# Performance work log

Hardware: AMD Instinct MI355X
Metric: run time of the kernel (lower is better)

Reference implementation:

```python
import jax, jax.numpy as jnp
import numpy as np
import math
from itertools import combinations

SEQ_LEN = 8
SET_SIZE = 3
IN_DIM = 2048
OUT_DIM = 1152
WAY = 5
SHOT = 5
N_QUERIES = 200
PE_SCALE = 0.1
LN_EPS = 1e-5
NEG_INF = -1e30

TUPLES = np.array(list(combinations(range(SEQ_LEN), SET_SIZE)), dtype=np.int32)  # [56, 3]
TUPLES_LEN = TUPLES.shape[0]


def _positional_encoding(d_model, max_len):
    position = np.arange(max_len)[:, None].astype(np.float32)
    div_term = np.exp(np.arange(0, d_model, 2).astype(np.float32) * -(math.log(10000.0) / d_model))
    pe = np.zeros((max_len, d_model), dtype=np.float32)
    pe[:, 0::2] = np.sin(position * div_term) * PE_SCALE
    pe[:, 1::2] = np.cos(position * div_term) * PE_SCALE
    return jnp.asarray(pe)

PE = _positional_encoding(IN_DIM, int(SEQ_LEN * 1.5))


def setup_inputs() -> dict:
    key = jax.random.key(0)
    ks = jax.random.split(key, 6)
    support_set = jax.random.normal(ks[0], (WAY * SHOT, SEQ_LEN, IN_DIM), dtype=jnp.float32)
    queries = jax.random.normal(ks[1], (N_QUERIES, SEQ_LEN, IN_DIM), dtype=jnp.float32)
    support_labels = jnp.repeat(jnp.arange(WAY, dtype=jnp.int32), SHOT)  # [25]
    Wk = jax.random.normal(ks[2], (IN_DIM * SET_SIZE, OUT_DIM), dtype=jnp.float32) * 0.02
    bk = jnp.zeros((OUT_DIM,), dtype=jnp.float32)
    Wv = jax.random.normal(ks[3], (IN_DIM * SET_SIZE, OUT_DIM), dtype=jnp.float32) * 0.02
    bv = jnp.zeros((OUT_DIM,), dtype=jnp.float32)
    ln_g = jnp.ones((OUT_DIM,), dtype=jnp.float32)
    ln_b = jnp.zeros((OUT_DIM,), dtype=jnp.float32)
    return {"support_set": support_set, "support_labels": support_labels, "queries": queries,
            "Wk": Wk, "bk": bk, "Wv": Wv, "bv": bv, "ln_g": ln_g, "ln_b": ln_b}


def _layernorm(x, g, b):
    mu = jnp.mean(x, axis=-1, keepdims=True)
    var = jnp.var(x, axis=-1, keepdims=True)
    return (x - mu) * jax.lax.rsqrt(var + LN_EPS) * g + b


def _tuple_features(x):
    # x: [N, SEQ_LEN, IN_DIM]; add PE (dropout is identity at inference), gather frame tuples.
    n = x.shape[0]
    x = x + PE[None, :x.shape[1], :]
    return x[:, TUPLES, :].reshape(n, TUPLES_LEN, SET_SIZE * IN_DIM)  # [N, 56, 6144]


def reference(support_set, support_labels, queries, Wk, bk, Wv, bv, ln_g, ln_b):
    n_q = queries.shape[0]
    s_feat = _tuple_features(support_set)   # [S, T, 6144]
    q_feat = _tuple_features(queries)       # [Q, T, 6144]

    sk = _layernorm(s_feat @ Wk + bk, ln_g, ln_b)  # [S, T, D]
    qk = _layernorm(q_feat @ Wk + bk, ln_g, ln_b)  # [Q, T, D]
    sv = s_feat @ Wv + bv                           # [S, T, D]
    qv = q_feat @ Wv + bv                           # [Q, T, D]

    # scores between every query tuple and every support tuple
    scores = jnp.einsum('qtd,skd->qtsk', qk, sk) / math.sqrt(OUT_DIM)  # [Q, T, S, T]

    # per-class masked softmax over (support clips of class c) x (support tuples)
    class_mask = support_labels[None, :] == jnp.arange(WAY, dtype=support_labels.dtype)[:, None]  # [WAY, S]
    masked = scores[None] + jnp.where(class_mask[:, None, None, :, None], 0.0, NEG_INF)  # [WAY, Q, T, S, T]
    attn = jax.nn.softmax(masked.reshape(WAY, n_q, TUPLES_LEN, -1), axis=-1)
    attn = attn.reshape(WAY, n_q, TUPLES_LEN, -1, TUPLES_LEN)  # [WAY, Q, T, S, T]

    proto = jnp.einsum('cqtsk,skd->cqtd', attn, sv)  # [WAY, Q, T, D]
    diff = qv[None] - proto                           # [WAY, Q, T, D]
    dist = -jnp.sum(diff * diff, axis=(2, 3)) / TUPLES_LEN  # [WAY, Q]
    return dist.T  # logits [Q, WAY]
```

## Files before the change

kernel.cpp:

```cpp
#include <hip/hip_runtime.h>
#include <math.h>

#define SEQ_LEN 8
#define IN_DIM 2048
#define OUT_DIM 1152
#define NTUP 56
#define NSUP 25
#define NQ 200
#define WAY 5
#define SFRAMES 200
#define NFRAMES 1800
#define SROWS 1400
#define QROWS 11200
#define AT_STRIDE 1440
#define KC 288
#define ALD 296

typedef __attribute__((ext_vector_type(8))) short short8;
typedef __attribute__((ext_vector_type(4))) float f32x4;

__device__ __constant__ int TUP[NTUP][3] = {
{0,1,2},{0,1,3},{0,1,4},{0,1,5},{0,1,6},{0,1,7},
{0,2,3},{0,2,4},{0,2,5},{0,2,6},{0,2,7},
{0,3,4},{0,3,5},{0,3,6},{0,3,7},
{0,4,5},{0,4,6},{0,4,7},
{0,5,6},{0,5,7},
{0,6,7},
{1,2,3},{1,2,4},{1,2,5},{1,2,6},{1,2,7},
{1,3,4},{1,3,5},{1,3,6},{1,3,7},
{1,4,5},{1,4,6},{1,4,7},
{1,5,6},{1,5,7},
{1,6,7},
{2,3,4},{2,3,5},{2,3,6},{2,3,7},
{2,4,5},{2,4,6},{2,4,7},
{2,5,6},{2,5,7},
{2,6,7},
{3,4,5},{3,4,6},{3,4,7},
{3,5,6},{3,5,7},
{3,6,7},
{4,5,6},{4,5,7},
{4,6,7},
{5,6,7}};

__device__ __forceinline__ unsigned short f2bf(float x) {
  union { float f; unsigned int u; } v; v.f = x;
  unsigned int r = v.u + 0x7fffu + ((v.u >> 16) & 1u);
  return (unsigned short)(r >> 16);
}
__device__ __forceinline__ float bf2f(unsigned short s) {
  union { float f; unsigned int u; } v; v.u = ((unsigned int)s) << 16;
  return v.f;
}

__device__ __forceinline__ void gll16(const void* g, void* l) {
  __builtin_amdgcn_global_load_lds(
      (const __attribute__((address_space(1))) unsigned int*)g,
      (__attribute__((address_space(3))) unsigned int*)l, 16, 0, 0);
}

#define VMCNT(N) asm volatile("s_waitcnt vmcnt(" #N ")" ::: "memory")

__device__ __forceinline__ void pbar() {
  asm volatile("" ::: "memory");
  __builtin_amdgcn_s_barrier();
  asm volatile("" ::: "memory");
}

#define APB_OFF   0UL
#define WT_OFF    7372800UL
#define PB_OFF    35684352UL
#define QKB_OFF   60567552UL
#define SKB_OFF   86372352UL
#define QVB_OFF   89597952UL
#define SVB_OFF   115402752UL
#define G2_OFF    118628352UL
#define SCB_OFF   119457792UL
#define G1B_OFF   151713792UL
#define QNORM_OFF 183969792UL
#define RANK_OFF  184014592UL

__global__ __launch_bounds__(256) void k_pre(const float* __restrict__ S,
                                             const float* __restrict__ Q,
                                             const float* __restrict__ Wk,
                                             const float* __restrict__ Wv,
                                             const int* __restrict__ labels,
                                             unsigned short* __restrict__ APb,
                                             unsigned short* __restrict__ WT,
                                             int* __restrict__ rank,
                                             float* __restrict__ outz) {
  __shared__ float t[32][33];
  int b = blockIdx.x, tid = threadIdx.x;
  if (b < NFRAMES) {
    int frame = b;
    int e8 = tid * 8;
    int pos = frame & 7;
    const float c0 = -logf(10000.0f) / (float)IN_DIM;
    float pe[8];
#pragma unroll
    for (int p = 0; p < 4; ++p) {
      float dt = expf((float)(e8 + 2 * p) * c0);
      float arg = (float)pos * dt;
      pe[2 * p] = sinf(arg) * 0.1f;
      pe[2 * p + 1] = cosf(arg) * 0.1f;
    }
    const float* src = (frame < SFRAMES) ? (S + (size_t)frame * IN_DIM + e8)
                                         : (Q + (size_t)(frame - SFRAMES) * IN_DIM + e8);
    float4 x0 = ((const float4*)src)[0], x1 = ((const float4*)src)[1];
    short8 o;
    o[0] = (short)f2bf(x0.x + pe[0]); o[1] = (short)f2bf(x0.y + pe[1]);
    o[2] = (short)f2bf(x0.z + pe[2]); o[3] = (short)f2bf(x0.w + pe[3]);
    o[4] = (short)f2bf(x1.x + pe[4]); o[5] = (short)f2bf(x1.y + pe[5]);
    o[6] = (short)f2bf(x1.z + pe[6]); o[7] = (short)f2bf(x1.w + pe[7]);
    *(short8*)(APb + (size_t)frame * IN_DIM + e8) = o;
  } else if (b < NFRAMES + 13824) {
    int z = b - NFRAMES;
    int bz = z / (64 * 36); int rem = z % (64 * 36);
    int by = rem / 64, bx = rem % 64;
    int w = bz / 3, j = bz % 3;
    const float* W = w ? Wv : Wk;
    int k0 = bx * 32, d0 = by * 32;
    int tx = tid & 31, ty = tid >> 5;
#pragma unroll
    for (int i = 0; i < 4; ++i) {
      int k = k0 + ty + i * 8;
      t[ty + i * 8][tx] = W[(size_t)(j * IN_DIM + k) * OUT_DIM + d0 + tx];
    }
    __syncthreads();
    int colbase = w * 3456 + j * 1152 + d0;
#pragma unroll
    for (int i = 0; i < 4; ++i) {
      int d = ty + i * 8;
      WT[(size_t)(colbase + d) * IN_DIM + k0 + tx] = f2bf(t[tx][d]);
    }
  } else {
    for (int i = tid; i < NQ * WAY; i += 256) outz[i] = 0.f;
    if (tid == 0) {
      for (int s = 0; s < NSUP; ++s) {
        int r = 0;
        for (int s2 = 0; s2 < NSUP; ++s2)
          r += (labels[s2] < labels[s]) || (labels[s2] == labels[s] && s2 < s);
        rank[s] = r;
      }
    }
  }
}

__device__ __forceinline__ void mfma_core256(const short* __restrict__ A, int lda, int maxA,
                                             const short* __restrict__ B, int ldb, int maxB,
                                             int K, short* lds, f32x4 (&acc)[8][4]) {
  int tid = threadIdx.x;
  int lane = tid & 63, wave = tid >> 6;
  int wm = wave >> 1, wn = wave & 1;
  int col = lane & 15, quad = lane >> 4;
  int kq8 = (quad ^ ((col >> 1) & 3)) * 8;

  int rt_ = tid >> 2;
  int qo = ((tid & 3) ^ ((tid >> 3) & 3)) * 8;
  const short* a0p = A + (size_t)min(rt_,       maxA) * lda + qo;
  const short* a1p = A + (size_t)min(rt_ + 64,  maxA) * lda + qo;
  const short* a2p = A + (size_t)min(rt_ + 128, maxA) * lda + qo;
  const short* a3p = A + (size_t)min(rt_ + 192, maxA) * lda + qo;
  const short* b0p = B + (size_t)min(rt_,       maxB) * ldb + qo;
  const short* b1p = B + (size_t)min(rt_ + 64,  maxB) * ldb + qo;
  const int nt = K >> 5;

#define STAGE(t)                                     \
  do {                                               \
    short* buf_ = lds + (((t) & 1) * 12288);         \
    int k0_ = (t) << 5;                              \
    gll16(a0p + k0_, buf_ + (size_t)tid * 8);        \
    gll16(a1p + k0_, buf_ + (size_t)(tid + 256) * 8);\
    gll16(a2p + k0_, buf_ + (size_t)(tid + 512) * 8);\
    gll16(a3p + k0_, buf_ + (size_t)(tid + 768) * 8);\
    gll16(b0p + k0_, buf_ + 8192 + (size_t)tid * 8); \
    gll16(b1p + k0_, buf_ + 8192 + (size_t)(tid + 256) * 8);\
  } while (0)

  STAGE(0);
  for (int t = 0; t < nt; ++t) {
    if (t + 1 < nt) { STAGE(t + 1); VMCNT(6); }
    else            { VMCNT(0); }
    pbar();
    const short* As = lds + ((t & 1) * 12288);
    const short* Bs = As + 8192;
    short8 af[8], bf[4];
#pragma unroll
    for (int i = 0; i < 8; ++i)
      af[i] = *(const short8*)(As + (wm * 128 + i * 16 + col) * 32 + kq8);
#pragma unroll
    for (int j = 0; j < 4; ++j)
      bf[j] = *(const short8*)(Bs + (wn * 64 + j * 16 + col) * 32 + kq8);
    __builtin_amdgcn_s_setprio(1);
#pragma unroll
    for (int i = 0; i < 8; ++i)
#pragma unroll
      for (int j = 0; j < 4; ++j)
        acc[i][j] = __builtin_amdgcn_mfma_f32_16x16x32_bf16(af[i], bf[j], acc[i][j], 0, 0, 0);
    __builtin_amdgcn_s_setprio(0);
    pbar();
  }
#undef STAGE
}

__global__ __launch_bounds__(256, 2) void k_gemm1(const unsigned short* __restrict__ APb,
                                                  const unsigned short* __restrict__ WT,
                                                  unsigned short* __restrict__ Pb) {
  __shared__ short lds[24576];
  int o = blockIdx.x;
  int L = (o & 7) * 54 + (o >> 3);
  int rt = L / 54, ct = L % 54;
  int row0 = rt << 8, col0 = ct << 7;
  f32x4 acc[8][4];
#pragma unroll
  for (int i = 0; i < 8; ++i)
#pragma unroll
    for (int j = 0; j < 4; ++j) acc[i][j] = (f32x4)(0.f);
  mfma_core256((const short*)APb + (size_t)row0 * IN_DIM, IN_DIM, min(255, NFRAMES - 1 - row0),
               (const short*)WT + (size_t)col0 * IN_DIM, IN_DIM, 127,
               IN_DIM, lds, acc);
  int lane = threadIdx.x & 63, wave = threadIdx.x >> 6;
  int wm = wave >> 1, wn = wave & 1, col = lane & 15, quad = lane >> 4;
#pragma unroll
  for (int i = 0; i < 8; ++i)
#pragma unroll
    for (int r = 0; r < 4; ++r) {
      int gr = row0 + wm * 128 + i * 16 + quad * 4 + r;
      if (gr >= NFRAMES) continue;
#pragma unroll
      for (int j = 0; j < 4; ++j)
        Pb[(size_t)gr * 6912 + col0 + wn * 64 + j * 16 + col] = f2bf(acc[i][j][r]);
    }
}

__global__ __launch_bounds__(256) void k_combine(const unsigned short* __restrict__ Pb,
                                                 const float* __restrict__ bk,
                                                 const float* __restrict__ bv,
                                                 const float* __restrict__ g,
                                                 const float* __restrict__ bb,
                                                 const int* __restrict__ rank,
                                                 unsigned short* __restrict__ SKb,
                                                 unsigned short* __restrict__ QKb,
                                                 unsigned short* __restrict__ SVb,
                                                 unsigned short* __restrict__ QVb,
                                                 float* __restrict__ qnorm) {
  __shared__ short L[8 * 3456];
  int n = blockIdx.x, w = blockIdx.y;
  int tid = threadIdx.x;
  bool sup = n < NSUP;
  int fbase = sup ? n * SEQ_LEN : SFRAMES + (n - NSUP) * SEQ_LEN;
  for (int i = 0; i < 14; ++i) {
    int idx = tid + 256 * i;
    if (idx < 3456) {
      int fr = idx / 432, off = (idx - fr * 432) * 8;
      *(short8*)(L + fr * 3456 + off) =
          *(const short8*)(Pb + (size_t)(fbase + fr) * 6912 + w * 3456 + off);
    }
  }
  __syncthreads();
  int wave = tid >> 6, lane = tid & 63;
  const float* bias = w ? bv : bk;
  float2 bi[9], gg[9], bbv[9];
#pragma unroll
  for (int i = 0; i < 9; ++i) {
    int p = lane + 64 * i;
    bi[i] = *(const float2*)(bias + 2 * p);
    if (w == 0) {
      gg[i] = *(const float2*)(g + 2 * p);
      bbv[i] = *(const float2*)(bb + 2 * p);
    }
  }
  int obase = sup ? rank[n] * NTUP : (n - NSUP) * NTUP;
  const unsigned int* Lu = (const unsigned int*)L;
  for (int t = wave; t < NTUP; t += 4) {
    int b0 = (TUP[t][0] * 3456) >> 1;
    int b1 = (TUP[t][1] * 3456 + 1152) >> 1;
    int b2 = (TUP[t][2] * 3456 + 2304) >> 1;
    float va[18];
    float sum = 0.f, sq = 0.f;
#pragma unroll
    for (int i = 0; i < 9; ++i) {
      int p = lane + 64 * i;
      unsigned int u0 = Lu[b0 + p], u1 = Lu[b1 + p], u2 = Lu[b2 + p];
      float a = bf2f((unsigned short)u0) + bf2f((unsigned short)u1) +
                bf2f((unsigned short)u2) + bi[i].x;
      float b = bf2f((unsigned short)(u0 >> 16)) + bf2f((unsigned short)(u1 >> 16)) +
                bf2f((unsigned short)(u2 >> 16)) + bi[i].y;
      va[2 * i] = a; va[2 * i + 1] = b;
      sum += a + b;
      sq += a * a + b * b;
    }
#pragma unroll
    for (int o = 32; o; o >>= 1) {
      sum += __shfl_xor(sum, o);
      sq += __shfl_xor(sq, o);
    }
    int orow = obase + t;
    if (w == 0) {
      float mean = sum * (1.f / OUT_DIM);
      float var = sq * (1.f / OUT_DIM) - mean * mean;
      float inv = rsqrtf(var + 1e-5f);
      unsigned short* outp = (sup ? SKb : QKb) + (size_t)orow * OUT_DIM;
#pragma unroll
      for (int i = 0; i < 9; ++i) {
        int p = lane + 64 * i;
        unsigned int lo = f2bf((va[2 * i] - mean) * inv * gg[i].x + bbv[i].x);
        unsigned int hi = f2bf((va[2 * i + 1] - mean) * inv * gg[i].y + bbv[i].y);
        *(unsigned int*)(outp + 2 * p) = lo | (hi << 16);
      }
    } else {
      unsigned short* outp = (sup ? SVb : QVb) + (size_t)orow * OUT_DIM;
#pragma unroll
      for (int i = 0; i < 9; ++i) {
        int p = lane + 64 * i;
        unsigned int lo = f2bf(va[2 * i]);
        unsigned int hi = f2bf(va[2 * i + 1]);
        *(unsigned int*)(outp + 2 * p) = lo | (hi << 16);
      }
      if (!sup && lane == 0) qnorm[orow] = sq;
    }
  }
}

__global__ __launch_bounds__(256, 2) void k_rowgemm(const unsigned short* __restrict__ QKb,
                                                    const unsigned short* __restrict__ SKb,
                                                    const unsigned short* __restrict__ QVb,
                                                    const unsigned short* __restrict__ SVb,
                                                    unsigned short* __restrict__ SCb,
                                                    unsigned short* __restrict__ G1b,
                                                    unsigned short* __restrict__ G2) {
  __shared__ short lds[24576];
  int o = blockIdx.x;
  int xcd = o & 7, idx = o >> 3;
  int L = (xcd < 6 ? xcd * 125 : 750 + (xcd - 6) * 124) + idx;
  f32x4 acc[8][4];
#pragma unroll
  for (int i = 0; i < 8; ++i)
#pragma unroll
    for (int j = 0; j < 4; ++j) acc[i][j] = (f32x4)(0.f);
  int lane = threadIdx.x & 63, wave = threadIdx.x >> 6;
  int wm = wave >> 1, wn = wave & 1, col = lane & 15, quad = lane >> 4;

  if (L < 968) {
    int g1 = L >= 484; int l = g1 ? L - 484 : L;
    int rt = l / 11, ct = l % 11;
    int row0 = rt << 8, col0 = ct << 7;
    const unsigned short* Am = g1 ? QVb : QKb;
    const unsigned short* Bm = g1 ? SVb : SKb;
    mfma_core256((const short*)Am + (size_t)row0 * OUT_DIM, OUT_DIM, min(255, QROWS - 1 - row0),
                 (const short*)Bm + (size_t)col0 * OUT_DIM, OUT_DIM, min(127, SROWS - 1 - col0),
                 OUT_DIM, lds, acc);
    unsigned short* outp = g1 ? G1b : SCb;
    const float scl = g1 ? 1.0f : 0.029462782549439483f;
#pragma unroll
    for (int i = 0; i < 8; ++i)
#pragma unroll
      for (int r = 0; r < 4; ++r) {
        int gr = row0 + wm * 128 + i * 16 + quad * 4 + r;
        if (gr >= QROWS) continue;
#pragma unroll
        for (int j = 0; j < 4; ++j) {
          int gc = col0 + wn * 64 + j * 16 + col;
          if (gc < SROWS) {
            int c = gc / 280;
            outp[(size_t)gr * AT_STRIDE + gc + c * 8] = f2bf(acc[i][j][r] * scl);
          }
        }
      }
  } else {
    int l = L - 968;
    int c = l / 6, rem = l % 6;
    int rt = rem / 3, ct = rem % 3;
    int i0 = rt << 8, j0 = ct << 7;
    const short* base = (const short*)SVb + (size_t)c * 280 * OUT_DIM;
    mfma_core256(base + (size_t)i0 * OUT_DIM, OUT_DIM, 279 - i0,
                 base + (size_t)j0 * OUT_DIM, OUT_DIM, min(127, 279 - j0),
                 OUT_DIM, lds, acc);
    unsigned short* g2c = G2 + (size_t)c * KC * KC;
#pragma unroll
    for (int i = 0; i < 8; ++i)
#pragma unroll
      for (int r = 0; r < 4; ++r) {
        int gi = i0 + wm * 128 + i * 16 + quad * 4 + r;
        if (gi >= KC) continue;
#pragma unroll
        for (int j = 0; j < 4; ++j) {
          int gj = j0 + wn * 64 + j * 16 + col;
          if (gj < KC) g2c[(size_t)gi * KC + gj] = f2bf(acc[i][j][r]);
        }
      }
  }
}

__global__ __launch_bounds__(256) void k_attn(const unsigned short* __restrict__ SCb,
                                              const unsigned short* __restrict__ G1b,
                                              const unsigned short* __restrict__ G2,
                                              const float* __restrict__ qnorm,
                                              float* __restrict__ out) {
  __shared__ short attn[64 * ALD];
  __shared__ short Bs[64 * KC];
  __shared__ float T2n[64];
  __shared__ float Sarr[64];
  __shared__ float rowsum[64];
  __shared__ float val[64];
  int r0 = blockIdx.x * 64, c = blockIdx.y;
  int tid = threadIdx.x;

  int lr = tid >> 2, h = tid & 3;
  const unsigned short* ps = SCb + (size_t)(r0 + lr) * AT_STRIDE + c * KC;
  const unsigned short* pg = G1b + (size_t)(r0 + lr) * AT_STRIDE + c * KC;
  short8 sv[9];
  float mx = -INFINITY;
#pragma unroll
  for (int i = 0; i < 9; ++i) {
    int v = h * 9 + i;
    if (v < 35) {
      sv[i] = *(const short8*)(ps + v * 8);
#pragma unroll
      for (int j = 0; j < 8; ++j) mx = fmaxf(mx, bf2f((unsigned short)sv[i][j]));
    }
  }
  mx = fmaxf(mx, __shfl_xor(mx, 1));
  mx = fmaxf(mx, __shfl_xor(mx, 2));
  float sum = 0.f, t2 = 0.f;
#pragma unroll
  for (int i = 0; i < 9; ++i) {
    int v = h * 9 + i;
    if (v < 35) {
      short8 gv8 = *(const short8*)(pg + v * 8);
      short8 e8;
#pragma unroll
      for (int j = 0; j < 8; ++j) {
        float e = __expf(bf2f((unsigned short)sv[i][j]) - mx);
        sum += e;
        t2 += e * bf2f((unsigned short)gv8[j]);
        e8[j] = (short)f2bf(e);
      }
      *(short8*)(attn + lr * ALD + v * 8) = e8;
    } else {
      *(short8*)(attn + lr * ALD + v * 8) = (short8)0;
    }
  }
  sum += __shfl_xor(sum, 1); sum += __shfl_xor(sum, 2);
  t2 += __shfl_xor(t2, 1); t2 += __shfl_xor(t2, 2);
  if (h == 0) { Sarr[lr] = sum; T2n[lr] = t2; }
  if (tid < 64) rowsum[tid] = 0.f;
  __syncthreads();

  int lane = tid & 63, wave = tid >> 6;
  int col = lane & 15, quad = lane >> 4;
  const short* G2c = (const short*)G2 + (size_t)c * KC * KC;
  float part[4][4] = {};
  for (int j0 = 0; j0 < KC; j0 += 64) {
    int ncols = min(64, KC - j0);
    int chunks = ncols * 36;
    for (int base = 0; base < chunks; base += 256) {
      int idx = base + tid;
      if (idx < chunks) {
        int n = idx / 36, kk = idx - n * 36;
        gll16(G2c + (size_t)(j0 + n) * KC + kk * 8, Bs + idx * 8);
      }
    }
    __syncthreads();
    if (wave * 16 < ncols) {
      f32x4 acc[4];
#pragma unroll
      for (int i = 0; i < 4; ++i) acc[i] = (f32x4)(0.f);
      for (int kq = 0; kq < 9; ++kq) {
        short8 bf = *(const short8*)(Bs + (wave * 16 + col) * KC + kq * 32 + quad * 8);
#pragma unroll
        for (int i = 0; i < 4; ++i) {
          short8 af = *(const short8*)(attn + (i * 16 + col) * ALD + kq * 32 + quad * 8);
          acc[i] = __builtin_amdgcn_mfma_f32_16x16x32_bf16(af, bf, acc[i], 0, 0, 0);
        }
      }
      int gcol = j0 + wave * 16 + col;
#pragma unroll
      for (int i = 0; i < 4; ++i)
#pragma unroll
        for (int r = 0; r < 4; ++r)
          part[i][r] += bf2f((unsigned short)attn[(i * 16 + quad * 4 + r) * ALD + gcol]) *
                        acc[i][r];
    }
    __syncthreads();
  }
#pragma unroll
  for (int i = 0; i < 4; ++i)
#pragma unroll
    for (int r = 0; r < 4; ++r) {
      float s = part[i][r];
      s += __shfl_xor(s, 1); s += __shfl_xor(s, 2);
      s += __shfl_xor(s, 4); s += __shfl_xor(s, 8);
      if (col == 0) atomicAdd(&rowsum[i * 16 + quad * 4 + r], s);
    }
  __syncthreads();

  if (tid < 64) {
    float S = Sarr[tid], invS = 1.f / S;
    val[tid] = qnorm[r0 + tid] - 2.f * T2n[tid] * invS + rowsum[tid] * invS * invS;
  }
  __syncthreads();
  if (tid < 3) {
    int q = r0 / NTUP + tid;
    int lo = max(q * NTUP, r0), hi = min(q * NTUP + NTUP, r0 + 64);
    if (lo < hi && q < NQ) {
      float s = 0.f;
      for (int r = lo; r < hi; ++r) s += val[r - r0];
      atomicAdd(&out[q * WAY + c], -s * (1.f / NTUP));
    }
  }
}

extern "C" void kernel_launch(void* const* d_in, const int* in_sizes, int n_in,
                              void* d_out, int out_size, void* d_ws, size_t ws_size,
                              hipStream_t stream) {
  const float* support = (const float*)d_in[0];
  const int* labels = (const int*)d_in[1];
  const float* queries = (const float*)d_in[2];
  const float* Wk = (const float*)d_in[3];
  const float* bk = (const float*)d_in[4];
  const float* Wv = (const float*)d_in[5];
  const float* bv = (const float*)d_in[6];
  const float* ln_g = (const float*)d_in[7];
  const float* ln_b = (const float*)d_in[8];
  float* out = (float*)d_out;
  char* w8 = (char*)d_ws;

  unsigned short* APb = (unsigned short*)(w8 + APB_OFF);
  unsigned short* WT = (unsigned short*)(w8 + WT_OFF);
  unsigned short* Pb = (unsigned short*)(w8 + PB_OFF);
  unsigned short* QKb = (unsigned short*)(w8 + QKB_OFF);
  unsigned short* SKb = (unsigned short*)(w8 + SKB_OFF);
  unsigned short* QVb = (unsigned short*)(w8 + QVB_OFF);
  unsigned short* SVb = (unsigned short*)(w8 + SVB_OFF);
  unsigned short* G2 = (unsigned short*)(w8 + G2_OFF);
  unsigned short* SCb = (unsigned short*)(w8 + SCB_OFF);
  unsigned short* G1b = (unsigned short*)(w8 + G1B_OFF);
  float* QNORM = (float*)(w8 + QNORM_OFF);
  int* RANK = (int*)(w8 + RANK_OFF);

  k_pre<<<dim3(NFRAMES + 13824 + 1), dim3(256), 0, stream>>>(support, queries, Wk, Wv,
                                                             labels, APb, WT, RANK, out);
  k_gemm1<<<dim3(432), dim3(256), 0, stream>>>(APb, WT, Pb);
  k_combine<<<dim3(225, 2), dim3(256), 0, stream>>>(Pb, bk, bv, ln_g, ln_b, RANK,
                                                    SKb, QKb, SVb, QVb, QNORM);
  k_rowgemm<<<dim3(998), dim3(256), 0, stream>>>(QKb, SKb, QVb, SVb, SCb, G1b, G2);
  k_attn<<<dim3(175, 5), dim3(256), 0, stream>>>(SCb, G1b, G2, QNORM, out);
}
```

Measured before the change: 348.5 us.

## Switch GEMMs to 256x256 tiles with 8 waves and interleaved LDS staging

```diff
diff --git a/kernel.cpp b/kernel.cpp
--- a/kernel.cpp
+++ b/kernel.cpp
@@ -145,81 +145,118 @@
   }
 }
 
-__device__ __forceinline__ void mfma_core256(const short* __restrict__ A, int lda, int maxA,
-                                             const short* __restrict__ B, int ldb, int maxB,
-                                             int K, short* lds, f32x4 (&acc)[8][4]) {
-  int tid = threadIdx.x;
-  int lane = tid & 63, wave = tid >> 6;
-  int wm = wave >> 1, wn = wave & 1;
-  int col = lane & 15, quad = lane >> 4;
-  int kq8 = (quad ^ ((col >> 1) & 3)) * 8;
-
-  int rt_ = tid >> 2;
-  int qo = ((tid & 3) ^ ((tid >> 3) & 3)) * 8;
-  const short* a0p = A + (size_t)min(rt_,       maxA) * lda + qo;
-  const short* a1p = A + (size_t)min(rt_ + 64,  maxA) * lda + qo;
-  const short* a2p = A + (size_t)min(rt_ + 128, maxA) * lda + qo;
-  const short* a3p = A + (size_t)min(rt_ + 192, maxA) * lda + qo;
-  const short* b0p = B + (size_t)min(rt_,       maxB) * ldb + qo;
-  const short* b1p = B + (size_t)min(rt_ + 64,  maxB) * ldb + qo;
-  const int nt = K >> 5;
-
-#define STAGE(t)                                     \
-  do {                                               \
-    short* buf_ = lds + (((t) & 1) * 12288);         \
-    int k0_ = (t) << 5;                              \
-    gll16(a0p + k0_, buf_ + (size_t)tid * 8);        \
-    gll16(a1p + k0_, buf_ + (size_t)(tid + 256) * 8);\
-    gll16(a2p + k0_, buf_ + (size_t)(tid + 512) * 8);\
-    gll16(a3p + k0_, buf_ + (size_t)(tid + 768) * 8);\
-    gll16(b0p + k0_, buf_ + 8192 + (size_t)tid * 8); \
-    gll16(b1p + k0_, buf_ + 8192 + (size_t)(tid + 256) * 8);\
-  } while (0)
-
-  STAGE(0);
+__device__ __forceinline__ void mfma_core8p(const short* __restrict__ A, int lda, int maxA,
+                                            const short* __restrict__ B, int ldb, int maxB,
+                                            int K, short* lds, f32x4 (&acc)[8][4]) {
+  const int tid = threadIdx.x;
+  const int lane = tid & 63, wave = tid >> 6;
+  const int wm = wave >> 2, wn = wave & 3;
+  const int col = lane & 15, quad = lane >> 4;
+  const int kq8 = (quad ^ ((col >> 1) & 3)) * 8;
+  const int arow = (wm * 128 + col) * 32 + kq8;
+  const int brow = (wn * 64 + col) * 32 + kq8;
+  const int r_ = tid >> 2;
+  const int qsrc = ((tid & 3) ^ ((tid >> 3) & 3)) * 8;
+  const short* aLo = A + (size_t)min(r_,       maxA) * lda + qsrc;
+  const short* aHi = A + (size_t)min(r_ + 128, maxA) * lda + qsrc;
+  const short* bLo = B + (size_t)min(r_,       maxB) * ldb + qsrc;
+  const short* bHi = B + (size_t)min(r_ + 128, maxB) * ldb + qsrc;
+  const int dst0 = tid * 8, dst1 = (tid + 512) * 8;
+  const int nt = K >> 6;
+
+#define STAGE_U(srcLo, srcHi, kk, base)                  \
+  do { gll16((srcLo) + (kk), lds + (base) + dst0);       \
+       gll16((srcHi) + (kk), lds + (base) + dst1); } while (0)
+
+  STAGE_U(aLo, aHi, 0, 0);
+  STAGE_U(bLo, bHi, 0, 16384);
+  STAGE_U(aLo, aHi, 32, 8192);
+  STAGE_U(bLo, bHi, 32, 24576);
+  VMCNT(4);
+  pbar();
+
   for (int t = 0; t < nt; ++t) {
-    if (t + 1 < nt) { STAGE(t + 1); VMCNT(6); }
-    else            { VMCNT(0); }
-    pbar();
-    const short* As = lds + ((t & 1) * 12288);
-    const short* Bs = As + 8192;
-    short8 af[8], bf[4];
-#pragma unroll
-    for (int i = 0; i < 8; ++i)
-      af[i] = *(const short8*)(As + (wm * 128 + i * 16 + col) * 32 + kq8);
-#pragma unroll
-    for (int j = 0; j < 4; ++j)
-      bf[j] = *(const short8*)(Bs + (wn * 64 + j * 16 + col) * 32 + kq8);
+    const int bb = (t & 1) << 15;
+    const int sb = ((t + 1) & 1) << 15;
+    const bool st = (t + 1 < nt);
+    const int kg = (t + 1) << 6;
+    short8 af[8], bf0, bf1;
+#pragma unroll
+    for (int i = 0; i < 8; ++i) af[i] = *(const short8*)(lds + bb + arow + i * 512);
+    bf0 = *(const short8*)(lds + bb + 16384 + brow);
+    bf1 = *(const short8*)(lds + bb + 16384 + brow + 512);
+    if (st) STAGE_U(aLo, aHi, kg, sb);
+    pbar();
     __builtin_amdgcn_s_setprio(1);
 #pragma unroll
-    for (int i = 0; i < 8; ++i)
-#pragma unroll
-      for (int j = 0; j < 4; ++j)
-        acc[i][j] = __builtin_amdgcn_mfma_f32_16x16x32_bf16(af[i], bf[j], acc[i][j], 0, 0, 0);
+    for (int i = 0; i < 8; ++i) {
+      acc[i][0] = __builtin_amdgcn_mfma_f32_16x16x32_bf16(af[i], bf0, acc[i][0], 0, 0, 0);
+      acc[i][1] = __builtin_amdgcn_mfma_f32_16x16x32_bf16(af[i], bf1, acc[i][1], 0, 0, 0);
+    }
     __builtin_amdgcn_s_setprio(0);
     pbar();
-  }
-#undef STAGE
-}
-
-__global__ __launch_bounds__(256, 2) void k_gemm1(const unsigned short* __restrict__ APb,
+    bf0 = *(const short8*)(lds + bb + 16384 + brow + 1024);
+    bf1 = *(const short8*)(lds + bb + 16384 + brow + 1536);
+    if (st) { STAGE_U(bLo, bHi, kg, sb + 16384); VMCNT(4); }
+    else    { VMCNT(0); }
+    pbar();
+    __builtin_amdgcn_s_setprio(1);
+#pragma unroll
+    for (int i = 0; i < 8; ++i) {
+      acc[i][2] = __builtin_amdgcn_mfma_f32_16x16x32_bf16(af[i], bf0, acc[i][2], 0, 0, 0);
+      acc[i][3] = __builtin_amdgcn_mfma_f32_16x16x32_bf16(af[i], bf1, acc[i][3], 0, 0, 0);
+    }
+    __builtin_amdgcn_s_setprio(0);
+    pbar();
+#pragma unroll
+    for (int i = 0; i < 8; ++i) af[i] = *(const short8*)(lds + bb + 8192 + arow + i * 512);
+    bf0 = *(const short8*)(lds + bb + 24576 + brow);
+    bf1 = *(const short8*)(lds + bb + 24576 + brow + 512);
+    if (st) STAGE_U(aLo, aHi, kg + 32, sb + 8192);
+    pbar();
+    __builtin_amdgcn_s_setprio(1);
+#pragma unroll
+    for (int i = 0; i < 8; ++i) {
+      acc[i][0] = __builtin_amdgcn_mfma_f32_16x16x32_bf16(af[i], bf0, acc[i][0], 0, 0, 0);
+      acc[i][1] = __builtin_amdgcn_mfma_f32_16x16x32_bf16(af[i], bf1, acc[i][1], 0, 0, 0);
+    }
+    __builtin_amdgcn_s_setprio(0);
+    pbar();
+    bf0 = *(const short8*)(lds + bb + 24576 + brow + 1024);
+    bf1 = *(const short8*)(lds + bb + 24576 + brow + 1536);
+    if (st) { STAGE_U(bLo, bHi, kg + 32, sb + 24576); VMCNT(4); }
+    else    { VMCNT(0); }
+    pbar();
+    __builtin_amdgcn_s_setprio(1);
+#pragma unroll
+    for (int i = 0; i < 8; ++i) {
+      acc[i][2] = __builtin_amdgcn_mfma_f32_16x16x32_bf16(af[i], bf0, acc[i][2], 0, 0, 0);
+      acc[i][3] = __builtin_amdgcn_mfma_f32_16x16x32_bf16(af[i], bf1, acc[i][3], 0, 0, 0);
+    }
+    __builtin_amdgcn_s_setprio(0);
+    pbar();
+  }
+#undef STAGE_U
+}
+
+__global__ __launch_bounds__(512, 2) void k_gemm1(const unsigned short* __restrict__ APb,
                                                   const unsigned short* __restrict__ WT,
                                                   unsigned short* __restrict__ Pb) {
-  __shared__ short lds[24576];
+  __shared__ short lds[65536];
   int o = blockIdx.x;
-  int L = (o & 7) * 54 + (o >> 3);
-  int rt = L / 54, ct = L % 54;
-  int row0 = rt << 8, col0 = ct << 7;
+  int L = (o & 7) * 27 + (o >> 3);
+  int rt = L / 27, ct = L % 27;
+  int row0 = rt << 8, col0 = ct << 8;
   f32x4 acc[8][4];
 #pragma unroll
   for (int i = 0; i < 8; ++i)
 #pragma unroll
     for (int j = 0; j < 4; ++j) acc[i][j] = (f32x4)(0.f);
-  mfma_core256((const short*)APb + (size_t)row0 * IN_DIM, IN_DIM, min(255, NFRAMES - 1 - row0),
-               (const short*)WT + (size_t)col0 * IN_DIM, IN_DIM, 127,
-               IN_DIM, lds, acc);
+  mfma_core8p((const short*)APb + (size_t)row0 * IN_DIM, IN_DIM, min(255, NFRAMES - 1 - row0),
+              (const short*)WT + (size_t)col0 * IN_DIM, IN_DIM, 255,
+              IN_DIM, lds, acc);
   int lane = threadIdx.x & 63, wave = threadIdx.x >> 6;
-  int wm = wave >> 1, wn = wave & 1, col = lane & 15, quad = lane >> 4;
+  int wm = wave >> 2, wn = wave & 3, col = lane & 15, quad = lane >> 4;
 #pragma unroll
   for (int i = 0; i < 8; ++i)
 #pragma unroll
@@ -321,34 +358,34 @@
   }
 }
 
-__global__ __launch_bounds__(256, 2) void k_rowgemm(const unsigned short* __restrict__ QKb,
+__global__ __launch_bounds__(512, 2) void k_rowgemm(const unsigned short* __restrict__ QKb,
                                                     const unsigned short* __restrict__ SKb,
                                                     const unsigned short* __restrict__ QVb,
                                                     const unsigned short* __restrict__ SVb,
                                                     unsigned short* __restrict__ SCb,
                                                     unsigned short* __restrict__ G1b,
                                                     unsigned short* __restrict__ G2) {
-  __shared__ short lds[24576];
+  __shared__ short lds[65536];
   int o = blockIdx.x;
   int xcd = o & 7, idx = o >> 3;
-  int L = (xcd < 6 ? xcd * 125 : 750 + (xcd - 6) * 124) + idx;
+  int L = (xcd < 4 ? xcd * 69 : 276 + (xcd - 4) * 68) + idx;
   f32x4 acc[8][4];
 #pragma unroll
   for (int i = 0; i < 8; ++i)
 #pragma unroll
     for (int j = 0; j < 4; ++j) acc[i][j] = (f32x4)(0.f);
   int lane = threadIdx.x & 63, wave = threadIdx.x >> 6;
-  int wm = wave >> 1, wn = wave & 1, col = lane & 15, quad = lane >> 4;
-
-  if (L < 968) {
-    int g1 = L >= 484; int l = g1 ? L - 484 : L;
-    int rt = l / 11, ct = l % 11;
-    int row0 = rt << 8, col0 = ct << 7;
+  int wm = wave >> 2, wn = wave & 3, col = lane & 15, quad = lane >> 4;
+
+  if (L < 528) {
+    int g1 = L >= 264; int l = g1 ? L - 264 : L;
+    int rt = l / 6, ct = l % 6;
+    int row0 = rt << 8, col0 = ct << 8;
     const unsigned short* Am = g1 ? QVb : QKb;
     const unsigned short* Bm = g1 ? SVb : SKb;
-    mfma_core256((const short*)Am + (size_t)row0 * OUT_DIM, OUT_DIM, min(255, QROWS - 1 - row0),
-                 (const short*)Bm + (size_t)col0 * OUT_DIM, OUT_DIM, min(127, SROWS - 1 - col0),
-                 OUT_DIM, lds, acc);
+    mfma_core8p((const short*)Am + (size_t)row0 * OUT_DIM, OUT_DIM, min(255, QROWS - 1 - row0),
+                (const short*)Bm + (size_t)col0 * OUT_DIM, OUT_DIM, min(255, SROWS - 1 - col0),
+                OUT_DIM, lds, acc);
     unsigned short* outp = g1 ? G1b : SCb;
     const float scl = g1 ? 1.0f : 0.029462782549439483f;
 #pragma unroll
@@ -367,14 +404,14 @@
         }
       }
   } else {
-    int l = L - 968;
-    int c = l / 6, rem = l % 6;
-    int rt = rem / 3, ct = rem % 3;
-    int i0 = rt << 8, j0 = ct << 7;
+    int l = L - 528;
+    int c = l >> 2, rem = l & 3;
+    int rt = rem >> 1, ct = rem & 1;
+    int i0 = rt << 8, j0 = ct << 8;
     const short* base = (const short*)SVb + (size_t)c * 280 * OUT_DIM;
-    mfma_core256(base + (size_t)i0 * OUT_DIM, OUT_DIM, 279 - i0,
-                 base + (size_t)j0 * OUT_DIM, OUT_DIM, min(127, 279 - j0),
-                 OUT_DIM, lds, acc);
+    mfma_core8p(base + (size_t)i0 * OUT_DIM, OUT_DIM, min(255, 279 - i0),
+                base + (size_t)j0 * OUT_DIM, OUT_DIM, min(255, 279 - j0),
+                OUT_DIM, lds, acc);
     unsigned short* g2c = G2 + (size_t)c * KC * KC;
 #pragma unroll
     for (int i = 0; i < 8; ++i)
@@ -540,9 +577,9 @@
 
   k_pre<<<dim3(NFRAMES + 13824 + 1), dim3(256), 0, stream>>>(support, queries, Wk, Wv,
                                                              labels, APb, WT, RANK, out);
-  k_gemm1<<<dim3(432), dim3(256), 0, stream>>>(APb, WT, Pb);
+  k_gemm1<<<dim3(216), dim3(512), 0, stream>>>(APb, WT, Pb);
   k_combine<<<dim3(225, 2), dim3(256), 0, stream>>>(Pb, bk, bv, ln_g, ln_b, RANK,
                                                     SKb, QKb, SVb, QVb, QNORM);
-  k_rowgemm<<<dim3(998), dim3(256), 0, stream>>>(QKb, SKb, QVb, SVb, SCb, G1b, G2);
+  k_rowgemm<<<dim3(548), dim3(512), 0, stream>>>(QKb, SKb, QVb, SVb, SCb, G1b, G2);
   k_attn<<<dim3(175, 5), dim3(256), 0, stream>>>(SCb, G1b, G2, QNORM, out);
 }
```

Result: slower. 369.3 us (+5.9%).

## Load B fragments directly to registers and triple-buffer A tiles in LDS

Applied to the files above, without the earlier changes.

```diff
diff --git a/kernel.cpp b/kernel.cpp
--- a/kernel.cpp
+++ b/kernel.cpp
@@ -160,49 +160,80 @@
   const short* a1p = A + (size_t)min(rt_ + 64,  maxA) * lda + qo;
   const short* a2p = A + (size_t)min(rt_ + 128, maxA) * lda + qo;
   const short* a3p = A + (size_t)min(rt_ + 192, maxA) * lda + qo;
-  const short* b0p = B + (size_t)min(rt_,       maxB) * ldb + qo;
-  const short* b1p = B + (size_t)min(rt_ + 64,  maxB) * ldb + qo;
+  const short* bp0 = B + (size_t)min(wn * 64 + col,      maxB) * ldb + quad * 8;
+  const short* bp1 = B + (size_t)min(wn * 64 + 16 + col, maxB) * ldb + quad * 8;
+  const short* bp2 = B + (size_t)min(wn * 64 + 32 + col, maxB) * ldb + quad * 8;
+  const short* bp3 = B + (size_t)min(wn * 64 + 48 + col, maxB) * ldb + quad * 8;
   const int nt = K >> 5;
 
-#define STAGE(t)                                     \
+#define STAGEA(t, cb)                                \
   do {                                               \
-    short* buf_ = lds + (((t) & 1) * 12288);         \
+    short* buf_ = lds + (cb);                        \
     int k0_ = (t) << 5;                              \
     gll16(a0p + k0_, buf_ + (size_t)tid * 8);        \
     gll16(a1p + k0_, buf_ + (size_t)(tid + 256) * 8);\
     gll16(a2p + k0_, buf_ + (size_t)(tid + 512) * 8);\
     gll16(a3p + k0_, buf_ + (size_t)(tid + 768) * 8);\
-    gll16(b0p + k0_, buf_ + 8192 + (size_t)tid * 8); \
-    gll16(b1p + k0_, buf_ + 8192 + (size_t)(tid + 256) * 8);\
   } while (0)
-
-  STAGE(0);
-  for (int t = 0; t < nt; ++t) {
-    if (t + 1 < nt) { STAGE(t + 1); VMCNT(6); }
-    else            { VMCNT(0); }
-    pbar();
-    const short* As = lds + ((t & 1) * 12288);
-    const short* Bs = As + 8192;
-    short8 af[8], bf[4];
-#pragma unroll
-    for (int i = 0; i < 8; ++i)
-      af[i] = *(const short8*)(As + (wm * 128 + i * 16 + col) * 32 + kq8);
-#pragma unroll
-    for (int j = 0; j < 4; ++j)
-      bf[j] = *(const short8*)(Bs + (wn * 64 + j * 16 + col) * 32 + kq8);
-    __builtin_amdgcn_s_setprio(1);
-#pragma unroll
-    for (int i = 0; i < 8; ++i)
-#pragma unroll
-      for (int j = 0; j < 4; ++j)
-        acc[i][j] = __builtin_amdgcn_mfma_f32_16x16x32_bf16(af[i], bf[j], acc[i][j], 0, 0, 0);
-    __builtin_amdgcn_s_setprio(0);
-    pbar();
-  }
-#undef STAGE
-}
-
-__global__ __launch_bounds__(256, 2) void k_gemm1(const unsigned short* __restrict__ APb,
+#define LOADB(dst, t)                                \
+  do {                                               \
+    int k0_ = (t) << 5;                              \
+    dst[0] = *(const short8*)(bp0 + k0_);            \
+    dst[1] = *(const short8*)(bp1 + k0_);            \
+    dst[2] = *(const short8*)(bp2 + k0_);            \
+    dst[3] = *(const short8*)(bp3 + k0_);            \
+  } while (0)
+#define MFMA16(BF)                                                                     \
+  do {                                                                                 \
+    short8 af[8];                                                                      \
+    _Pragma("unroll")                                                                  \
+    for (int i = 0; i < 8; ++i)                                                        \
+      af[i] = *(const short8*)(As + (wm * 128 + i * 16 + col) * 32 + kq8);             \
+    __builtin_amdgcn_s_setprio(1);                                                     \
+    _Pragma("unroll")                                                                  \
+    for (int i = 0; i < 8; ++i)                                                        \
+      _Pragma("unroll")                                                                \
+      for (int j = 0; j < 4; ++j)                                                      \
+        acc[i][j] = __builtin_amdgcn_mfma_f32_16x16x32_bf16(af[i], BF[j], acc[i][j],   \
+                                                            0, 0, 0);                  \
+    __builtin_amdgcn_s_setprio(0);                                                     \
+  } while (0)
+
+  short8 bfA[4], bfB[4];
+  LOADB(bfA, 0);
+  STAGEA(0, 0);
+  STAGEA(1, 8192);
+  VMCNT(4);
+  pbar();
+  int c0 = 0, c1 = 8192, c2 = 16384;
+  for (int t = 0; t < nt; t += 2) {
+    {
+      LOADB(bfB, t + 1);
+      if (t + 2 < nt) STAGEA(t + 2, c2);
+      const short* As = lds + c0;
+      MFMA16(bfA);
+      if (t + 2 < nt) { VMCNT(8); }
+      else            { VMCNT(4); }
+      pbar();
+      int tmp = c0; c0 = c1; c1 = c2; c2 = tmp;
+    }
+    {
+      int u = t + 1;
+      if (u + 1 < nt) LOADB(bfA, u + 1);
+      if (u + 2 < nt) STAGEA(u + 2, c2);
+      const short* As = lds + c0;
+      MFMA16(bfB);
+      if (u + 2 < nt)      { VMCNT(8); pbar(); }
+      else if (u + 1 < nt) { VMCNT(4); pbar(); }
+      int tmp = c0; c0 = c1; c1 = c2; c2 = tmp;
+    }
+  }
+#undef STAGEA
+#undef LOADB
+#undef MFMA16
+}
+
+__global__ __launch_bounds__(256, 3) void k_gemm1(const unsigned short* __restrict__ APb,
                                                   const unsigned short* __restrict__ WT,
                                                   unsigned short* __restrict__ Pb) {
   __shared__ short lds[24576];
@@ -321,7 +352,7 @@
   }
 }
 
-__global__ __launch_bounds__(256, 2) void k_rowgemm(const unsigned short* __restrict__ QKb,
+__global__ __launch_bounds__(256, 3) void k_rowgemm(const unsigned short* __restrict__ QKb,
                                                     const unsigned short* __restrict__ SKb,
                                                     const unsigned short* __restrict__ QVb,
                                                     const unsigned short* __restrict__ SVb,
```

After: 1.233 ms. 3.54x slower.
